# Performance work log

Hardware: AMD Instinct MI355X
Metric: run time of the kernel (lower is better)

The kernel has to match this reference:

```python
import jax, jax.numpy as jnp
import numpy as np

NIN, NHID, NDECHID, NOUT = 128, 256, 512, 10
B, N = 32, 4096


def _linear_params(key, fan_in, fan_out):
    kw, kb = jax.random.split(key)
    bound = 1.0 / np.sqrt(fan_in)
    W = jax.random.uniform(kw, (fan_in, fan_out), jnp.float32, -bound, bound)
    b = jax.random.uniform(kb, (fan_out,), jnp.float32, -bound, bound)
    return W, b


def setup_inputs() -> dict:
    key = jax.random.key(0)
    ks = jax.random.split(key, 7)
    x = jax.random.normal(ks[0], (B, N, NIN), jnp.float32)
    W1, b1 = _linear_params(ks[1], NIN, NHID)
    W2, b2 = _linear_params(ks[2], NHID, NHID)
    W3, b3 = _linear_params(ks[3], NHID, NHID)
    D1, c1 = _linear_params(ks[4], NHID, NDECHID)
    D2, c2 = _linear_params(ks[5], NDECHID, NDECHID)
    D3, c3 = _linear_params(ks[6], NDECHID, NOUT)
    return {"x": x, "W1": W1, "b1": b1, "W2": W2, "b2": b2, "W3": W3, "b3": b3,
            "D1": D1, "c1": c1, "D2": D2, "c2": c2, "D3": D3, "c3": c3}


def reference(x, W1, b1, W2, b2, W3, b3, D1, c1, D2, c2, D3, c3):
    # encoder MLP: Linear-ReLU-Linear-ReLU-Linear, then extra ReLU
    h = jax.nn.relu(x @ W1 + b1)            # [B, N, nhid]
    h = jax.nn.relu(h @ W2 + b2)
    h = jax.nn.relu(h @ W3 + b3)            # fused enc output + F.relu
    # mean_{i,j}(h_i * h_j) over the set == (mean_i h)^2 elementwise (exact identity)
    m = jnp.mean(h, axis=1)                  # [B, nhid]
    p = jax.nn.relu(m * m)                   # [B, nhid]
    # decoder MLP
    d = jax.nn.relu(p @ D1 + c1)
    d = jax.nn.relu(d @ D2 + c2)
    return d @ D3 + c3                       # [B, nout]
```

## Files before the change

kernel.cpp:

```cpp
#include <hip/hip_runtime.h>
#include <hip/hip_bf16.h>
#include <stdint.h>


#define NIN   128
#define NHID  256
#define NDEC  512
#define NOUTC 10
#define BATCH 32
#define NTOK  4096
#define MTILE 64
#define NBLK  (BATCH * (NTOK / MTILE))

#define SWZ(t) (((t) & 7) << 4)

typedef short bf16x8 __attribute__((ext_vector_type(8)));
typedef float floatx4 __attribute__((ext_vector_type(4)));

__device__ __forceinline__ uint16_t f2b(float f) {
  union { uint32_t u; float f; } v; v.f = f;
  uint32_t r = v.u + 0x7FFFu + ((v.u >> 16) & 1u);
  return (uint16_t)(r >> 16);
}
__device__ __forceinline__ uint32_t pkbf(float lo, float hi) {
  __hip_bfloat162 h = __float22bfloat162_rn(float2{lo, hi});
  union { __hip_bfloat162 h; uint32_t u; } c; c.h = h;
  return c.u;
}

__global__ __launch_bounds__(256) void pack_weights(
    const float* __restrict__ W1, const float* __restrict__ W2,
    const float* __restrict__ W3, const float* __restrict__ c3,
    uint16_t* __restrict__ pW, float* __restrict__ msum,
    float* __restrict__ out) {
  int p = blockIdx.x * blockDim.x + threadIdx.x;
  if (p < BATCH * NHID) msum[p] = 0.f;
  if (p < BATCH * NOUTC) out[p] = c3[p % NOUTC];
  const float* W; int K; int base;
  if (p < 32768)      { W = W1; K = NIN;  base = 0; }
  else if (p < 98304) { W = W2; K = NHID; base = 32768; p -= 32768; }
  else                { W = W3; K = NHID; base = 98304; p -= 98304; }
  int j    = p & 7;
  int ln   = (p >> 3) & 63;
  int rest = p >> 9;
  int KC = K >> 5;
  int kc = rest % KC;
  int mt = rest / KC;
  int m = mt * 16 + (ln & 15);
  int k = kc * 32 + ((ln >> 4) << 3) + j;
  pW[base + (((mt * KC + kc) * 64 + ln) << 3) + j] = f2b(W[k * NHID + m]);
}

__global__ __launch_bounds__(256) void encoder(
    const float* __restrict__ x,
    const uint16_t* __restrict__ pW,
    const float* __restrict__ b1,
    const float* __restrict__ b2,
    const float* __restrict__ b3,
    float* __restrict__ msum) {
  __shared__ __align__(16) uint8_t Hs[MTILE * 512];

  const int tid  = threadIdx.x;
  const int wave = tid >> 6;
  const int lane = tid & 63;
  const int l15  = lane & 15;
  const int q    = lane >> 4;
  const int tok0  = blockIdx.x * MTILE;
  const int batch = blockIdx.x >> 6;

  const uint16_t* pW1 = pW;
  const uint16_t* pW2 = pW + 32768;
  const uint16_t* pW3 = pW + 98304;

  {
    const float4* xv = (const float4*)(x + (size_t)tok0 * NIN);
#pragma unroll
    for (int i = 0; i < 4; ++i) {
      const int u = tid + i * 256;
      float4 va = xv[2 * u];
      float4 vb = xv[2 * u + 1];
      uint4 w = make_uint4(pkbf(va.x, va.y), pkbf(va.z, va.w),
                           pkbf(vb.x, vb.y), pkbf(vb.z, vb.w));
      const int row = u >> 4;
      const int cb  = (u & 15) << 4;
      *(uint4*)&Hs[row * 256 + (cb ^ SWZ(row))] = w;
    }
  }
  __syncthreads();

  floatx4 acc[4][4];

#pragma unroll
  for (int jt = 0; jt < 4; ++jt) {
    const float4 bb = *(const float4*)&b1[wave * 64 + jt * 16 + q * 4];
#pragma unroll
    for (int tt = 0; tt < 4; ++tt)
      acc[jt][tt] = (floatx4){bb.x, bb.y, bb.z, bb.w};
  }
#pragma unroll
  for (int kc = 0; kc < 4; ++kc) {
    bf16x8 a[4], b[4];
#pragma unroll
    for (int jt = 0; jt < 4; ++jt)
      a[jt] = *(const bf16x8*)(pW1 + ((((wave * 4 + jt) * 4 + kc) * 64 + lane) << 3));
#pragma unroll
    for (int tt = 0; tt < 4; ++tt) {
      const int t = tt * 16 + l15;
      b[tt] = *(const bf16x8*)&Hs[t * 256 + ((kc * 64 + q * 16) ^ SWZ(t))];
    }
#pragma unroll
    for (int jt = 0; jt < 4; ++jt)
#pragma unroll
      for (int tt = 0; tt < 4; ++tt)
        acc[jt][tt] = __builtin_amdgcn_mfma_f32_16x16x32_bf16(
            a[jt], b[tt], acc[jt][tt], 0, 0, 0);
  }
  __syncthreads();

#pragma unroll
  for (int jt = 0; jt < 4; ++jt) {
    const int cb = (wave * 64 + jt * 16 + q * 4) * 2;
#pragma unroll
    for (int tt = 0; tt < 4; ++tt) {
      const int t = tt * 16 + l15;
      float v0 = fmaxf(acc[jt][tt][0], 0.f);
      float v1 = fmaxf(acc[jt][tt][1], 0.f);
      float v2 = fmaxf(acc[jt][tt][2], 0.f);
      float v3 = fmaxf(acc[jt][tt][3], 0.f);
      *(uint2*)&Hs[t * 512 + (cb ^ SWZ(t))] = make_uint2(pkbf(v0, v1), pkbf(v2, v3));
    }
  }
  __syncthreads();

#pragma unroll
  for (int jt = 0; jt < 4; ++jt) {
    const float4 bb = *(const float4*)&b2[wave * 64 + jt * 16 + q * 4];
#pragma unroll
    for (int tt = 0; tt < 4; ++tt)
      acc[jt][tt] = (floatx4){bb.x, bb.y, bb.z, bb.w};
  }
#pragma unroll
  for (int kc = 0; kc < 8; ++kc) {
    bf16x8 a[4], b[4];
#pragma unroll
    for (int jt = 0; jt < 4; ++jt)
      a[jt] = *(const bf16x8*)(pW2 + ((((wave * 4 + jt) * 8 + kc) * 64 + lane) << 3));
#pragma unroll
    for (int tt = 0; tt < 4; ++tt) {
      const int t = tt * 16 + l15;
      b[tt] = *(const bf16x8*)&Hs[t * 512 + ((kc * 64 + q * 16) ^ SWZ(t))];
    }
#pragma unroll
    for (int jt = 0; jt < 4; ++jt)
#pragma unroll
      for (int tt = 0; tt < 4; ++tt)
        acc[jt][tt] = __builtin_amdgcn_mfma_f32_16x16x32_bf16(
            a[jt], b[tt], acc[jt][tt], 0, 0, 0);
  }
  __syncthreads();
#pragma unroll
  for (int jt = 0; jt < 4; ++jt) {
    const int cb = (wave * 64 + jt * 16 + q * 4) * 2;
#pragma unroll
    for (int tt = 0; tt < 4; ++tt) {
      const int t = tt * 16 + l15;
      float v0 = fmaxf(acc[jt][tt][0], 0.f);
      float v1 = fmaxf(acc[jt][tt][1], 0.f);
      float v2 = fmaxf(acc[jt][tt][2], 0.f);
      float v3 = fmaxf(acc[jt][tt][3], 0.f);
      *(uint2*)&Hs[t * 512 + (cb ^ SWZ(t))] = make_uint2(pkbf(v0, v1), pkbf(v2, v3));
    }
  }
  __syncthreads();

#pragma unroll
  for (int jt = 0; jt < 4; ++jt) {
    const float4 bb = *(const float4*)&b3[wave * 64 + jt * 16 + q * 4];
#pragma unroll
    for (int tt = 0; tt < 4; ++tt)
      acc[jt][tt] = (floatx4){bb.x, bb.y, bb.z, bb.w};
  }
#pragma unroll
  for (int kc = 0; kc < 8; ++kc) {
    bf16x8 a[4], b[4];
#pragma unroll
    for (int jt = 0; jt < 4; ++jt)
      a[jt] = *(const bf16x8*)(pW3 + ((((wave * 4 + jt) * 8 + kc) * 64 + lane) << 3));
#pragma unroll
    for (int tt = 0; tt < 4; ++tt) {
      const int t = tt * 16 + l15;
      b[tt] = *(const bf16x8*)&Hs[t * 512 + ((kc * 64 + q * 16) ^ SWZ(t))];
    }
#pragma unroll
    for (int jt = 0; jt < 4; ++jt)
#pragma unroll
      for (int tt = 0; tt < 4; ++tt)
        acc[jt][tt] = __builtin_amdgcn_mfma_f32_16x16x32_bf16(
            a[jt], b[tt], acc[jt][tt], 0, 0, 0);
  }
  __syncthreads();

  {
    float4* scratch = (float4*)Hs;
#pragma unroll
    for (int jt = 0; jt < 4; ++jt) {
      float s0 = 0.f, s1 = 0.f, s2 = 0.f, s3 = 0.f;
#pragma unroll
      for (int tt = 0; tt < 4; ++tt) {
        s0 += fmaxf(acc[jt][tt][0], 0.f);
        s1 += fmaxf(acc[jt][tt][1], 0.f);
        s2 += fmaxf(acc[jt][tt][2], 0.f);
        s3 += fmaxf(acc[jt][tt][3], 0.f);
      }
      scratch[((wave * 4 + jt) * 4 + q) * 17 + l15] = (float4){s0, s1, s2, s3};
    }
  }
  __syncthreads();
  {
    const int c = tid >> 2;
    const int r = tid & 3;
    const float* sf = (const float*)Hs;
    float v = 0.f;
#pragma unroll
    for (int l = 0; l < 16; ++l)
      v += sf[c * 68 + l * 4 + r];
    const int wv = c >> 4, jt = (c >> 2) & 3, qq = c & 3;
    const int j = wv * 64 + jt * 16 + qq * 4 + r;
    atomicAdd(&msum[batch * NHID + j], v);
  }
}

__global__ __launch_bounds__(1024) void decoder(
    const float* __restrict__ msum,
    const float* __restrict__ D1, const float* __restrict__ c1,
    const float* __restrict__ D2, const float* __restrict__ c2,
    const float* __restrict__ D3,
    float* __restrict__ out) {
  __shared__ float p[NHID];
  __shared__ float d1[NDEC];
  __shared__ float d2q[128];
  __shared__ __align__(16) float red[4096];
  const int b = blockIdx.x >> 2, qd = blockIdx.x & 3, t = threadIdx.x;

  if (t < NHID) {
    float m = msum[b * NHID + t] * (1.f / NTOK);
    p[t] = m * m;
  }
  __syncthreads();

  {
    const int jg = t & 127;
    const int ks = t >> 7;
    const float4* D1v = (const float4*)D1;
    float4 s = {0.f, 0.f, 0.f, 0.f};
    for (int k = ks * 32; k < ks * 32 + 32; ++k) {
      float4 w = D1v[k * 128 + jg];
      float pv = p[k];
      s.x += pv * w.x; s.y += pv * w.y; s.z += pv * w.z; s.w += pv * w.w;
    }
    *(float4*)&red[t * 4] = s;
    __syncthreads();
    if (t < NDEC) {
      float v = c1[t];
#pragma unroll
      for (int i = 0; i < 8; ++i) v += red[i * 512 + t];
      d1[t] = fmaxf(v, 0.f);
    }
    __syncthreads();
  }

  {
    const int jg2 = t & 31;
    const int ks2 = t >> 5;
    const float4* D2v = (const float4*)D2;
    float4 s = {0.f, 0.f, 0.f, 0.f};
    for (int k = ks2 * 16; k < ks2 * 16 + 16; ++k) {
      float4 w = D2v[k * 128 + qd * 32 + jg2];
      float hv = d1[k];
      s.x += hv * w.x; s.y += hv * w.y; s.z += hv * w.z; s.w += hv * w.w;
    }
    *(float4*)&red[t * 4] = s;
    __syncthreads();
    if (t < 128) {
      float v = c2[qd * 128 + t];
#pragma unroll
      for (int i = 0; i < 32; ++i) v += red[i * 128 + t];
      d2q[t] = fmaxf(v, 0.f);
    }
    __syncthreads();
  }

  {
    const int j3 = t & 15;
    const int kc = t >> 4;
    float s = 0.f;
    if (j3 < NOUTC)
      for (int k = kc * 2; k < kc * 2 + 2; ++k)
        s += d2q[k] * D3[(qd * 128 + k) * NOUTC + j3];
    red[t] = s;
    __syncthreads();
    if (t < NOUTC) {
      float v = 0.f;
#pragma unroll
      for (int i = 0; i < 64; ++i) v += red[i * 16 + t];
      atomicAdd(&out[b * NOUTC + t], v);
    }
  }
}

extern "C" void kernel_launch(void* const* d_in, const int* in_sizes, int n_in,
                              void* d_out, int out_size, void* d_ws, size_t ws_size,
                              hipStream_t stream) {
  const float* x  = (const float*)d_in[0];
  const float* W1 = (const float*)d_in[1];
  const float* b1 = (const float*)d_in[2];
  const float* W2 = (const float*)d_in[3];
  const float* b2 = (const float*)d_in[4];
  const float* W3 = (const float*)d_in[5];
  const float* b3 = (const float*)d_in[6];
  const float* D1 = (const float*)d_in[7];
  const float* c1 = (const float*)d_in[8];
  const float* D2 = (const float*)d_in[9];
  const float* c2 = (const float*)d_in[10];
  const float* D3 = (const float*)d_in[11];
  const float* c3 = (const float*)d_in[12];

  uint16_t* pW   = (uint16_t*)d_ws;
  float*    msum = (float*)((char*)d_ws + 384 * 1024);

  pack_weights<<<640, 256, 0, stream>>>(W1, W2, W3, c3, pW, msum,
                                        (float*)d_out);
  encoder<<<NBLK, 256, 0, stream>>>(x, pW, b1, b2, b3, msum);
  decoder<<<128, 1024, 0, stream>>>(msum, D1, c1, D2, c2, D3,
                                    (float*)d_out);
}
```

Measured before the change: 159.6 us.

## Repartition encoder waves by token rows and reduce column sums with shuffles

```diff
diff --git a/kernel.cpp b/kernel.cpp
--- a/kernel.cpp
+++ b/kernel.cpp
@@ -67,6 +67,7 @@
   const int q    = lane >> 4;
   const int tok0  = blockIdx.x * MTILE;
   const int batch = blockIdx.x >> 6;
+  const int trow  = wave * 16 + l15;
 
   const uint16_t* pW1 = pW;
   const uint16_t* pW2 = pW + 32768;
@@ -88,145 +89,124 @@
   }
   __syncthreads();
 
-  floatx4 acc[4][4];
-
-#pragma unroll
-  for (int jt = 0; jt < 4; ++jt) {
-    const float4 bb = *(const float4*)&b1[wave * 64 + jt * 16 + q * 4];
-#pragma unroll
-    for (int tt = 0; tt < 4; ++tt)
-      acc[jt][tt] = (floatx4){bb.x, bb.y, bb.z, bb.w};
+  floatx4 acc[16];
+
+#pragma unroll
+  for (int jt = 0; jt < 16; ++jt) {
+    const float4 bb = *(const float4*)&b1[jt * 16 + q * 4];
+    acc[jt] = (floatx4){bb.x, bb.y, bb.z, bb.w};
   }
 #pragma unroll
   for (int kc = 0; kc < 4; ++kc) {
-    bf16x8 a[4], b[4];
-#pragma unroll
-    for (int jt = 0; jt < 4; ++jt)
-      a[jt] = *(const bf16x8*)(pW1 + ((((wave * 4 + jt) * 4 + kc) * 64 + lane) << 3));
-#pragma unroll
-    for (int tt = 0; tt < 4; ++tt) {
-      const int t = tt * 16 + l15;
-      b[tt] = *(const bf16x8*)&Hs[t * 256 + ((kc * 64 + q * 16) ^ SWZ(t))];
-    }
-#pragma unroll
-    for (int jt = 0; jt < 4; ++jt)
-#pragma unroll
-      for (int tt = 0; tt < 4; ++tt)
-        acc[jt][tt] = __builtin_amdgcn_mfma_f32_16x16x32_bf16(
-            a[jt], b[tt], acc[jt][tt], 0, 0, 0);
-  }
-  __syncthreads();
-
-#pragma unroll
-  for (int jt = 0; jt < 4; ++jt) {
-    const int cb = (wave * 64 + jt * 16 + q * 4) * 2;
-#pragma unroll
-    for (int tt = 0; tt < 4; ++tt) {
-      const int t = tt * 16 + l15;
-      float v0 = fmaxf(acc[jt][tt][0], 0.f);
-      float v1 = fmaxf(acc[jt][tt][1], 0.f);
-      float v2 = fmaxf(acc[jt][tt][2], 0.f);
-      float v3 = fmaxf(acc[jt][tt][3], 0.f);
-      *(uint2*)&Hs[t * 512 + (cb ^ SWZ(t))] = make_uint2(pkbf(v0, v1), pkbf(v2, v3));
-    }
-  }
-  __syncthreads();
-
-#pragma unroll
-  for (int jt = 0; jt < 4; ++jt) {
-    const float4 bb = *(const float4*)&b2[wave * 64 + jt * 16 + q * 4];
-#pragma unroll
-    for (int tt = 0; tt < 4; ++tt)
-      acc[jt][tt] = (floatx4){bb.x, bb.y, bb.z, bb.w};
+    bf16x8 b = *(const bf16x8*)&Hs[trow * 256 + ((kc * 64 + q * 16) ^ SWZ(trow))];
+#pragma unroll
+    for (int jc = 0; jc < 4; ++jc) {
+      bf16x8 a0 = *(const bf16x8*)(pW1 + ((((jc * 4 + 0) * 4 + kc) * 64 + lane) << 3));
+      bf16x8 a1 = *(const bf16x8*)(pW1 + ((((jc * 4 + 1) * 4 + kc) * 64 + lane) << 3));
+      bf16x8 a2 = *(const bf16x8*)(pW1 + ((((jc * 4 + 2) * 4 + kc) * 64 + lane) << 3));
+      bf16x8 a3 = *(const bf16x8*)(pW1 + ((((jc * 4 + 3) * 4 + kc) * 64 + lane) << 3));
+      acc[jc * 4 + 0] = __builtin_amdgcn_mfma_f32_16x16x32_bf16(a0, b, acc[jc * 4 + 0], 0, 0, 0);
+      acc[jc * 4 + 1] = __builtin_amdgcn_mfma_f32_16x16x32_bf16(a1, b, acc[jc * 4 + 1], 0, 0, 0);
+      acc[jc * 4 + 2] = __builtin_amdgcn_mfma_f32_16x16x32_bf16(a2, b, acc[jc * 4 + 2], 0, 0, 0);
+      acc[jc * 4 + 3] = __builtin_amdgcn_mfma_f32_16x16x32_bf16(a3, b, acc[jc * 4 + 3], 0, 0, 0);
+    }
+  }
+  __syncthreads();
+
+#pragma unroll
+  for (int jt = 0; jt < 16; ++jt) {
+    const int cb = jt * 32 + q * 8;
+    float v0 = fmaxf(acc[jt][0], 0.f);
+    float v1 = fmaxf(acc[jt][1], 0.f);
+    float v2 = fmaxf(acc[jt][2], 0.f);
+    float v3 = fmaxf(acc[jt][3], 0.f);
+    *(uint2*)&Hs[trow * 512 + (cb ^ SWZ(trow))] = make_uint2(pkbf(v0, v1), pkbf(v2, v3));
+  }
+  __syncthreads();
+
+#pragma unroll
+  for (int jt = 0; jt < 16; ++jt) {
+    const float4 bb = *(const float4*)&b2[jt * 16 + q * 4];
+    acc[jt] = (floatx4){bb.x, bb.y, bb.z, bb.w};
   }
 #pragma unroll
   for (int kc = 0; kc < 8; ++kc) {
-    bf16x8 a[4], b[4];
-#pragma unroll
-    for (int jt = 0; jt < 4; ++jt)
-      a[jt] = *(const bf16x8*)(pW2 + ((((wave * 4 + jt) * 8 + kc) * 64 + lane) << 3));
-#pragma unroll
-    for (int tt = 0; tt < 4; ++tt) {
-      const int t = tt * 16 + l15;
-      b[tt] = *(const bf16x8*)&Hs[t * 512 + ((kc * 64 + q * 16) ^ SWZ(t))];
-    }
-#pragma unroll
-    for (int jt = 0; jt < 4; ++jt)
-#pragma unroll
-      for (int tt = 0; tt < 4; ++tt)
-        acc[jt][tt] = __builtin_amdgcn_mfma_f32_16x16x32_bf16(
-            a[jt], b[tt], acc[jt][tt], 0, 0, 0);
-  }
-  __syncthreads();
-#pragma unroll
-  for (int jt = 0; jt < 4; ++jt) {
-    const int cb = (wave * 64 + jt * 16 + q * 4) * 2;
-#pragma unroll
-    for (int tt = 0; tt < 4; ++tt) {
-      const int t = tt * 16 + l15;
-      float v0 = fmaxf(acc[jt][tt][0], 0.f);
-      float v1 = fmaxf(acc[jt][tt][1], 0.f);
-      float v2 = fmaxf(acc[jt][tt][2], 0.f);
-      float v3 = fmaxf(acc[jt][tt][3], 0.f);
-      *(uint2*)&Hs[t * 512 + (cb ^ SWZ(t))] = make_uint2(pkbf(v0, v1), pkbf(v2, v3));
-    }
-  }
-  __syncthreads();
-
-#pragma unroll
-  for (int jt = 0; jt < 4; ++jt) {
-    const float4 bb = *(const float4*)&b3[wave * 64 + jt * 16 + q * 4];
-#pragma unroll
-    for (int tt = 0; tt < 4; ++tt)
-      acc[jt][tt] = (floatx4){bb.x, bb.y, bb.z, bb.w};
+    bf16x8 b = *(const bf16x8*)&Hs[trow * 512 + ((kc * 64 + q * 16) ^ SWZ(trow))];
+#pragma unroll
+    for (int jc = 0; jc < 4; ++jc) {
+      bf16x8 a0 = *(const bf16x8*)(pW2 + ((((jc * 4 + 0) * 8 + kc) * 64 + lane) << 3));
+      bf16x8 a1 = *(const bf16x8*)(pW2 + ((((jc * 4 + 1) * 8 + kc) * 64 + lane) << 3));
+      bf16x8 a2 = *(const bf16x8*)(pW2 + ((((jc * 4 + 2) * 8 + kc) * 64 + lane) << 3));
+      bf16x8 a3 = *(const bf16x8*)(pW2 + ((((jc * 4 + 3) * 8 + kc) * 64 + lane) << 3));
+      acc[jc * 4 + 0] = __builtin_amdgcn_mfma_f32_16x16x32_bf16(a0, b, acc[jc * 4 + 0], 0, 0, 0);
+      acc[jc * 4 + 1] = __builtin_amdgcn_mfma_f32_16x16x32_bf16(a1, b, acc[jc * 4 + 1], 0, 0, 0);
+      acc[jc * 4 + 2] = __builtin_amdgcn_mfma_f32_16x16x32_bf16(a2, b, acc[jc * 4 + 2], 0, 0, 0);
+      acc[jc * 4 + 3] = __builtin_amdgcn_mfma_f32_16x16x32_bf16(a3, b, acc[jc * 4 + 3], 0, 0, 0);
+    }
+  }
+  __syncthreads();
+#pragma unroll
+  for (int jt = 0; jt < 16; ++jt) {
+    const int cb = jt * 32 + q * 8;
+    float v0 = fmaxf(acc[jt][0], 0.f);
+    float v1 = fmaxf(acc[jt][1], 0.f);
+    float v2 = fmaxf(acc[jt][2], 0.f);
+    float v3 = fmaxf(acc[jt][3], 0.f);
+    *(uint2*)&Hs[trow * 512 + (cb ^ SWZ(trow))] = make_uint2(pkbf(v0, v1), pkbf(v2, v3));
+  }
+  __syncthreads();
+
+#pragma unroll
+  for (int jt = 0; jt < 16; ++jt) {
+    const float4 bb = *(const float4*)&b3[jt * 16 + q * 4];
+    acc[jt] = (floatx4){bb.x, bb.y, bb.z, bb.w};
   }
 #pragma unroll
   for (int kc = 0; kc < 8; ++kc) {
-    bf16x8 a[4], b[4];
-#pragma unroll
-    for (int jt = 0; jt < 4; ++jt)
-      a[jt] = *(const bf16x8*)(pW3 + ((((wave * 4 + jt) * 8 + kc) * 64 + lane) << 3));
-#pragma unroll
-    for (int tt = 0; tt < 4; ++tt) {
-      const int t = tt * 16 + l15;
-      b[tt] = *(const bf16x8*)&Hs[t * 512 + ((kc * 64 + q * 16) ^ SWZ(t))];
-    }
-#pragma unroll
-    for (int jt = 0; jt < 4; ++jt)
-#pragma unroll
-      for (int tt = 0; tt < 4; ++tt)
-        acc[jt][tt] = __builtin_amdgcn_mfma_f32_16x16x32_bf16(
-            a[jt], b[tt], acc[jt][tt], 0, 0, 0);
+    bf16x8 b = *(const bf16x8*)&Hs[trow * 512 + ((kc * 64 + q * 16) ^ SWZ(trow))];
+#pragma unroll
+    for (int jc = 0; jc < 4; ++jc) {
+      bf16x8 a0 = *(const bf16x8*)(pW3 + ((((jc * 4 + 0) * 8 + kc) * 64 + lane) << 3));
+      bf16x8 a1 = *(const bf16x8*)(pW3 + ((((jc * 4 + 1) * 8 + kc) * 64 + lane) << 3));
+      bf16x8 a2 = *(const bf16x8*)(pW3 + ((((jc * 4 + 2) * 8 + kc) * 64 + lane) << 3));
+      bf16x8 a3 = *(const bf16x8*)(pW3 + ((((jc * 4 + 3) * 8 + kc) * 64 + lane) << 3));
+      acc[jc * 4 + 0] = __builtin_amdgcn_mfma_f32_16x16x32_bf16(a0, b, acc[jc * 4 + 0], 0, 0, 0);
+      acc[jc * 4 + 1] = __builtin_amdgcn_mfma_f32_16x16x32_bf16(a1, b, acc[jc * 4 + 1], 0, 0, 0);
+      acc[jc * 4 + 2] = __builtin_amdgcn_mfma_f32_16x16x32_bf16(a2, b, acc[jc * 4 + 2], 0, 0, 0);
+      acc[jc * 4 + 3] = __builtin_amdgcn_mfma_f32_16x16x32_bf16(a3, b, acc[jc * 4 + 3], 0, 0, 0);
+    }
+  }
+
+  float4 jsum[16];
+#pragma unroll
+  for (int jt = 0; jt < 16; ++jt) {
+    float s0 = fmaxf(acc[jt][0], 0.f);
+    float s1 = fmaxf(acc[jt][1], 0.f);
+    float s2 = fmaxf(acc[jt][2], 0.f);
+    float s3 = fmaxf(acc[jt][3], 0.f);
+#pragma unroll
+    for (int m = 1; m <= 8; m <<= 1) {
+      s0 += __shfl_xor(s0, m);
+      s1 += __shfl_xor(s1, m);
+      s2 += __shfl_xor(s2, m);
+      s3 += __shfl_xor(s3, m);
+    }
+    jsum[jt] = (float4){s0, s1, s2, s3};
   }
   __syncthreads();
 
   {
     float4* scratch = (float4*)Hs;
 #pragma unroll
-    for (int jt = 0; jt < 4; ++jt) {
-      float s0 = 0.f, s1 = 0.f, s2 = 0.f, s3 = 0.f;
-#pragma unroll
-      for (int tt = 0; tt < 4; ++tt) {
-        s0 += fmaxf(acc[jt][tt][0], 0.f);
-        s1 += fmaxf(acc[jt][tt][1], 0.f);
-        s2 += fmaxf(acc[jt][tt][2], 0.f);
-        s3 += fmaxf(acc[jt][tt][3], 0.f);
-      }
-      scratch[((wave * 4 + jt) * 4 + q) * 17 + l15] = (float4){s0, s1, s2, s3};
-    }
-  }
-  __syncthreads();
-  {
-    const int c = tid >> 2;
-    const int r = tid & 3;
+    for (int jt = 0; jt < 16; ++jt)
+      if (l15 == jt)
+        scratch[(wave * 16 + jt) * 4 + q] = jsum[jt];
+  }
+  __syncthreads();
+  if (tid < NHID) {
     const float* sf = (const float*)Hs;
-    float v = 0.f;
-#pragma unroll
-    for (int l = 0; l < 16; ++l)
-      v += sf[c * 68 + l * 4 + r];
-    const int wv = c >> 4, jt = (c >> 2) & 3, qq = c & 3;
-    const int j = wv * 64 + jt * 16 + qq * 4 + r;
-    atomicAdd(&msum[batch * NHID + j], v);
+    float v = sf[tid] + sf[256 + tid] + sf[512 + tid] + sf[768 + tid];
+    atomicAdd(&msum[batch * NHID + tid], v);
   }
 }
 
```

Result: slower. 283.2 us (+77.5%).

## Run encoder layers 2 and 3 in FP8 MFMA and reduce with shuffles

Applied to the files above, without the earlier changes.

```diff
diff --git a/kernel.cpp b/kernel.cpp
--- a/kernel.cpp
+++ b/kernel.cpp
@@ -31,34 +31,39 @@
 __global__ __launch_bounds__(256) void pack_weights(
     const float* __restrict__ W1, const float* __restrict__ W2,
     const float* __restrict__ W3, const float* __restrict__ c3,
-    uint16_t* __restrict__ pW, float* __restrict__ msum,
+    uint8_t* __restrict__ pW, float* __restrict__ msum,
     float* __restrict__ out) {
   int p = blockIdx.x * blockDim.x + threadIdx.x;
   if (p < BATCH * NHID) msum[p] = 0.f;
   if (p < BATCH * NOUTC) out[p] = c3[p % NOUTC];
-  const float* W; int K; int base;
-  if (p < 32768)      { W = W1; K = NIN;  base = 0; }
-  else if (p < 98304) { W = W2; K = NHID; base = 32768; p -= 32768; }
-  else                { W = W3; K = NHID; base = 98304; p -= 98304; }
-  int j    = p & 7;
-  int ln   = (p >> 3) & 63;
-  int rest = p >> 9;
-  int KC = K >> 5;
-  int kc = rest % KC;
-  int mt = rest / KC;
-  int m = mt * 16 + (ln & 15);
-  int k = kc * 32 + ((ln >> 4) << 3) + j;
-  pW[base + (((mt * KC + kc) * 64 + ln) << 3) + j] = f2b(W[k * NHID + m]);
+  if (p < 32768) {
+    int j = p & 7, ln = (p >> 3) & 63, rest = p >> 9;
+    int kc = rest & 3, mt = rest >> 2;
+    int m = mt * 16 + (ln & 15);
+    int k = kc * 32 + ((ln >> 4) << 3) + j;
+    ((uint16_t*)pW)[p] = f2b(W1[k * NHID + m]);
+  } else {
+    int p2 = p - 32768;
+    const float* W = (p2 < 65536) ? W2 : W3;
+    int base = (p2 < 65536) ? 65536 : 131072;
+    if (p2 >= 65536) p2 -= 65536;
+    int j = p2 & 7, ln = (p2 >> 3) & 63, rest = p2 >> 9;
+    int kc = rest & 7, mt = rest >> 3;
+    int m = mt * 16 + (ln & 15);
+    int k = kc * 32 + ((ln >> 4) << 3) + j;
+    int r = __builtin_amdgcn_cvt_pk_fp8_f32(W[k * NHID + m], 0.f, 0, false);
+    pW[base + p2] = (uint8_t)(r & 0xFF);
+  }
 }
 
 __global__ __launch_bounds__(256) void encoder(
     const float* __restrict__ x,
-    const uint16_t* __restrict__ pW,
+    const uint8_t* __restrict__ pW,
     const float* __restrict__ b1,
     const float* __restrict__ b2,
     const float* __restrict__ b3,
     float* __restrict__ msum) {
-  __shared__ __align__(16) uint8_t Hs[MTILE * 512];
+  __shared__ __align__(16) uint8_t Hs[MTILE * 256];
 
   const int tid  = threadIdx.x;
   const int wave = tid >> 6;
@@ -68,9 +73,9 @@
   const int tok0  = blockIdx.x * MTILE;
   const int batch = blockIdx.x >> 6;
 
-  const uint16_t* pW1 = pW;
-  const uint16_t* pW2 = pW + 32768;
-  const uint16_t* pW3 = pW + 98304;
+  const uint16_t* pW1 = (const uint16_t*)pW;
+  const uint8_t*  pW2 = pW + 65536;
+  const uint8_t*  pW3 = pW + 131072;
 
   {
     const float4* xv = (const float4*)(x + (size_t)tok0 * NIN);
@@ -119,7 +124,7 @@
 
 #pragma unroll
   for (int jt = 0; jt < 4; ++jt) {
-    const int cb = (wave * 64 + jt * 16 + q * 4) * 2;
+    const int j0 = wave * 64 + jt * 16 + q * 4;
 #pragma unroll
     for (int tt = 0; tt < 4; ++tt) {
       const int t = tt * 16 + l15;
@@ -127,7 +132,9 @@
       float v1 = fmaxf(acc[jt][tt][1], 0.f);
       float v2 = fmaxf(acc[jt][tt][2], 0.f);
       float v3 = fmaxf(acc[jt][tt][3], 0.f);
-      *(uint2*)&Hs[t * 512 + (cb ^ SWZ(t))] = make_uint2(pkbf(v0, v1), pkbf(v2, v3));
+      int u = __builtin_amdgcn_cvt_pk_fp8_f32(v0, v1, 0, false);
+      u = __builtin_amdgcn_cvt_pk_fp8_f32(v2, v3, u, true);
+      *(uint32_t*)&Hs[t * 256 + (j0 ^ SWZ(t))] = (uint32_t)u;
     }
   }
   __syncthreads();
@@ -141,26 +148,27 @@
   }
 #pragma unroll
   for (int kc = 0; kc < 8; ++kc) {
-    bf16x8 a[4], b[4];
-#pragma unroll
-    for (int jt = 0; jt < 4; ++jt)
-      a[jt] = *(const bf16x8*)(pW2 + ((((wave * 4 + jt) * 8 + kc) * 64 + lane) << 3));
-#pragma unroll
-    for (int tt = 0; tt < 4; ++tt) {
-      const int t = tt * 16 + l15;
-      b[tt] = *(const bf16x8*)&Hs[t * 512 + ((kc * 64 + q * 16) ^ SWZ(t))];
+    long a[4], b[4];
+#pragma unroll
+    for (int jt = 0; jt < 4; ++jt)
+      a[jt] = *(const long*)(pW2 + ((((wave * 4 + jt) * 8 + kc) * 64 + lane) << 3));
+#pragma unroll
+    for (int tt = 0; tt < 4; ++tt) {
+      const int t = tt * 16 + l15;
+      b[tt] = *(const long*)&Hs[t * 256 + ((kc * 32 + q * 8) ^ SWZ(t))];
     }
 #pragma unroll
     for (int jt = 0; jt < 4; ++jt)
 #pragma unroll
       for (int tt = 0; tt < 4; ++tt)
-        acc[jt][tt] = __builtin_amdgcn_mfma_f32_16x16x32_bf16(
+        acc[jt][tt] = __builtin_amdgcn_mfma_f32_16x16x32_fp8_fp8(
             a[jt], b[tt], acc[jt][tt], 0, 0, 0);
   }
   __syncthreads();
-#pragma unroll
-  for (int jt = 0; jt < 4; ++jt) {
-    const int cb = (wave * 64 + jt * 16 + q * 4) * 2;
+
+#pragma unroll
+  for (int jt = 0; jt < 4; ++jt) {
+    const int j0 = wave * 64 + jt * 16 + q * 4;
 #pragma unroll
     for (int tt = 0; tt < 4; ++tt) {
       const int t = tt * 16 + l15;
@@ -168,7 +176,9 @@
       float v1 = fmaxf(acc[jt][tt][1], 0.f);
       float v2 = fmaxf(acc[jt][tt][2], 0.f);
       float v3 = fmaxf(acc[jt][tt][3], 0.f);
-      *(uint2*)&Hs[t * 512 + (cb ^ SWZ(t))] = make_uint2(pkbf(v0, v1), pkbf(v2, v3));
+      int u = __builtin_amdgcn_cvt_pk_fp8_f32(v0, v1, 0, false);
+      u = __builtin_amdgcn_cvt_pk_fp8_f32(v2, v3, u, true);
+      *(uint32_t*)&Hs[t * 256 + (j0 ^ SWZ(t))] = (uint32_t)u;
     }
   }
   __syncthreads();
@@ -182,51 +192,46 @@
   }
 #pragma unroll
   for (int kc = 0; kc < 8; ++kc) {
-    bf16x8 a[4], b[4];
-#pragma unroll
-    for (int jt = 0; jt < 4; ++jt)
-      a[jt] = *(const bf16x8*)(pW3 + ((((wave * 4 + jt) * 8 + kc) * 64 + lane) << 3));
-#pragma unroll
-    for (int tt = 0; tt < 4; ++tt) {
-      const int t = tt * 16 + l15;
-      b[tt] = *(const bf16x8*)&Hs[t * 512 + ((kc * 64 + q * 16) ^ SWZ(t))];
+    long a[4], b[4];
+#pragma unroll
+    for (int jt = 0; jt < 4; ++jt)
+      a[jt] = *(const long*)(pW3 + ((((wave * 4 + jt) * 8 + kc) * 64 + lane) << 3));
+#pragma unroll
+    for (int tt = 0; tt < 4; ++tt) {
+      const int t = tt * 16 + l15;
+      b[tt] = *(const long*)&Hs[t * 256 + ((kc * 32 + q * 8) ^ SWZ(t))];
     }
 #pragma unroll
     for (int jt = 0; jt < 4; ++jt)
 #pragma unroll
       for (int tt = 0; tt < 4; ++tt)
-        acc[jt][tt] = __builtin_amdgcn_mfma_f32_16x16x32_bf16(
+        acc[jt][tt] = __builtin_amdgcn_mfma_f32_16x16x32_fp8_fp8(
             a[jt], b[tt], acc[jt][tt], 0, 0, 0);
   }
-  __syncthreads();
-
-  {
-    float4* scratch = (float4*)Hs;
-#pragma unroll
-    for (int jt = 0; jt < 4; ++jt) {
-      float s0 = 0.f, s1 = 0.f, s2 = 0.f, s3 = 0.f;
-#pragma unroll
-      for (int tt = 0; tt < 4; ++tt) {
-        s0 += fmaxf(acc[jt][tt][0], 0.f);
-        s1 += fmaxf(acc[jt][tt][1], 0.f);
-        s2 += fmaxf(acc[jt][tt][2], 0.f);
-        s3 += fmaxf(acc[jt][tt][3], 0.f);
-      }
-      scratch[((wave * 4 + jt) * 4 + q) * 17 + l15] = (float4){s0, s1, s2, s3};
-    }
-  }
-  __syncthreads();
-  {
-    const int c = tid >> 2;
-    const int r = tid & 3;
-    const float* sf = (const float*)Hs;
-    float v = 0.f;
-#pragma unroll
-    for (int l = 0; l < 16; ++l)
-      v += sf[c * 68 + l * 4 + r];
-    const int wv = c >> 4, jt = (c >> 2) & 3, qq = c & 3;
-    const int j = wv * 64 + jt * 16 + qq * 4 + r;
-    atomicAdd(&msum[batch * NHID + j], v);
+#pragma unroll
+  for (int jt = 0; jt < 4; ++jt) {
+    float s0 = 0.f, s1 = 0.f, s2 = 0.f, s3 = 0.f;
+#pragma unroll
+    for (int tt = 0; tt < 4; ++tt) {
+      s0 += fmaxf(acc[jt][tt][0], 0.f);
+      s1 += fmaxf(acc[jt][tt][1], 0.f);
+      s2 += fmaxf(acc[jt][tt][2], 0.f);
+      s3 += fmaxf(acc[jt][tt][3], 0.f);
+    }
+#pragma unroll
+    for (int m = 1; m <= 8; m <<= 1) {
+      s0 += __shfl_xor(s0, m);
+      s1 += __shfl_xor(s1, m);
+      s2 += __shfl_xor(s2, m);
+      s3 += __shfl_xor(s3, m);
+    }
+    if (l15 == 0) {
+      const int jb = batch * NHID + wave * 64 + jt * 16 + q * 4;
+      atomicAdd(&msum[jb + 0], s0);
+      atomicAdd(&msum[jb + 1], s1);
+      atomicAdd(&msum[jb + 2], s2);
+      atomicAdd(&msum[jb + 3], s3);
+    }
   }
 }
 
@@ -325,8 +330,8 @@
   const float* D3 = (const float*)d_in[11];
   const float* c3 = (const float*)d_in[12];
 
-  uint16_t* pW   = (uint16_t*)d_ws;
-  float*    msum = (float*)((char*)d_ws + 384 * 1024);
+  uint8_t* pW   = (uint8_t*)d_ws;
+  float*   msum = (float*)((char*)d_ws + 384 * 1024);
 
   pack_weights<<<640, 256, 0, stream>>>(W1, W2, W3, c3, pW, msum,
                                         (float*)d_out);
```

Result: slower. 171.2 us (+7.3%).
